# Performance work log

Measured on AMD Instinct MI355X. Metric: run time of the kernel, lower is better.

## Reference

```python
import jax, jax.numpy as jnp
import numpy as np

N = 50000   # nodes
E = 800000  # edges
D = 256     # input feature dim
H = 128     # hidden size
OUT = 40    # output classes


def setup_inputs() -> dict:
    key = jax.random.key(0)
    ks = jax.random.split(key, 10)
    s = 0.05
    return {
        "x": jax.random.normal(ks[0], (N, D), jnp.float32),
        "edge_index": jax.random.randint(ks[1], (2, E), 0, N, dtype=jnp.int64),
        "W0": jax.random.normal(ks[2], (D, H), jnp.float32) * s,
        "b0": jnp.zeros((H,), jnp.float32),
        "W1": jax.random.normal(ks[3], (H, H), jnp.float32) * s,
        "b1": jnp.zeros((H,), jnp.float32),
        "W2": jax.random.normal(ks[4], (H, H), jnp.float32) * s,
        "b2": jnp.zeros((H,), jnp.float32),
        "Wout": jax.random.normal(ks[5], (H * 3, OUT), jnp.float32) * s,
        "bout": jnp.zeros((OUT,), jnp.float32),
    }


def _gcn_norm(edge_index, n):
    # PyG gcn_norm: add self-loops, symmetric D^-1/2 (A+I) D^-1/2 weights
    row, col = edge_index[0], edge_index[1]
    loop = jnp.arange(n, dtype=edge_index.dtype)
    row = jnp.concatenate([row, loop])
    col = jnp.concatenate([col, loop])
    deg = jax.ops.segment_sum(jnp.ones_like(col, jnp.float32), col, num_segments=n)
    dinv = jnp.where(deg > 0, jax.lax.rsqrt(jnp.maximum(deg, 1.0)), 0.0)
    norm = dinv[row] * dinv[col]  # [E+N]
    return row, col, norm


def _gcn_conv(x, W, b, row, col, norm, n):
    h = x @ W                                   # dense transform first (PyG order)
    msg = h[row] * norm[:, None]                # gather source feats, scale
    out = jax.ops.segment_sum(msg, col, num_segments=n)  # scatter-aggregate
    return out + b


def reference(x, edge_index, W0, b0, W1, b1, W2, b2, Wout, bout):
    n = x.shape[0]
    row, col, norm = _gcn_norm(edge_index, n)
    x1 = jax.nn.relu(_gcn_conv(x, W0, b0, row, col, norm, n))
    x2 = jax.nn.relu(_gcn_conv(x1, W1, b1, row, col, norm, n))
    x3 = jax.nn.relu(_gcn_conv(x2, W2, b2, row, col, norm, n))
    xs = jnp.concatenate([x1, x2, x3], axis=-1)  # JumpingKnowledge 'cat'
    return xs @ Wout + bout
```

## Files before the change

kernel.cpp:

```cpp
#include <hip/hip_runtime.h>

#define HID 128
#define NOUT 40
#define SCAN_B 256

typedef __attribute__((ext_vector_type(8))) short bf16x8;
typedef __attribute__((ext_vector_type(4))) float f32x4;

__device__ inline float bf2f(unsigned short u) {
    unsigned int t = ((unsigned int)u) << 16;
    float f;
    __builtin_memcpy(&f, &t, 4);
    return f;
}
__device__ inline unsigned short f2bf(float f) {
    unsigned int x;
    __builtin_memcpy(&x, &f, 4);
    unsigned int r = (x + 0x7fffu + ((x >> 16) & 1u)) >> 16;
    return (unsigned short)r;
}
__device__ inline bf16x8 pack_bf8(float4 u, float4 v) {
    bf16x8 r;
    r[0] = (short)f2bf(u.x); r[1] = (short)f2bf(u.y);
    r[2] = (short)f2bf(u.z); r[3] = (short)f2bf(u.w);
    r[4] = (short)f2bf(v.x); r[5] = (short)f2bf(v.y);
    r[6] = (short)f2bf(v.z); r[7] = (short)f2bf(v.w);
    return r;
}

__global__ void detect_fmt_kernel(const unsigned int* __restrict__ e, int* __restrict__ flag) {
    int t = threadIdx.x;
    unsigned int v = e[2 * t + 1];
    unsigned long long ball = __ballot(v == 0u);
    if (t == 0) *flag = (ball == ~0ull) ? 1 : 0;
}

__global__ void convert_kernel(const void* __restrict__ eix, const int* __restrict__ flag,
                               int* __restrict__ rc, int* __restrict__ deg, int n2e) {
    int i = blockIdx.x * blockDim.x + threadIdx.x;
    if (i >= n2e) return;
    int f = *flag;
    int v;
    if (f) v = (int)(((const long long*)eix)[i]);
    else   v = ((const int*)eix)[i];
    rc[i] = v;
    if (i >= (n2e >> 1)) atomicAdd(&deg[v], 1);
}

__global__ void scan1_kernel(const int* __restrict__ deg, int* __restrict__ offs,
                             int* __restrict__ bsum, float* __restrict__ dinv, int N) {
    __shared__ int s[SCAN_B];
    int i = blockIdx.x * SCAN_B + threadIdx.x;
    int v = (i < N) ? deg[i] : 0;
    if (i < N) dinv[i] = rsqrtf((float)v + 1.0f);
    s[threadIdx.x] = v;
    __syncthreads();
    for (int d = 1; d < SCAN_B; d <<= 1) {
        int t = (threadIdx.x >= d) ? s[threadIdx.x - d] : 0;
        __syncthreads();
        s[threadIdx.x] += t;
        __syncthreads();
    }
    if (i < N) offs[i] = s[threadIdx.x] - v;
    if (threadIdx.x == SCAN_B - 1) bsum[blockIdx.x] = s[SCAN_B - 1];
}

__global__ void scan2_kernel(int* __restrict__ bsum, int nb) {
    __shared__ int s[SCAN_B];
    int v = (threadIdx.x < nb) ? bsum[threadIdx.x] : 0;
    s[threadIdx.x] = v;
    __syncthreads();
    for (int d = 1; d < SCAN_B; d <<= 1) {
        int t = (threadIdx.x >= d) ? s[threadIdx.x - d] : 0;
        __syncthreads();
        s[threadIdx.x] += t;
        __syncthreads();
    }
    if (threadIdx.x < nb) bsum[threadIdx.x] = s[threadIdx.x] - v;
}

__global__ void scan3_kernel(int* __restrict__ offs, const int* __restrict__ bsum,
                             int* __restrict__ cursor, int N, int E) {
    int i = blockIdx.x * SCAN_B + threadIdx.x;
    if (i < N) {
        int v = offs[i] + bsum[blockIdx.x];
        offs[i] = v;
        cursor[i] = v;
    }
    if (blockIdx.x == 0 && threadIdx.x == 0) offs[N] = E;
}

__global__ void fill_csr_kernel(const int* __restrict__ row, const int* __restrict__ col,
                                const float* __restrict__ dinv, int* __restrict__ cursor,
                                int* __restrict__ csrc, float* __restrict__ wgt, int E) {
    int e = blockIdx.x * blockDim.x + threadIdx.x;
    if (e >= E) return;
    int r = row[e];
    int c = col[e];
    int p = atomicAdd(&cursor[c], 1);
    csrc[p] = r;
    wgt[p] = dinv[r] * dinv[c];
}

__global__ void wt_kernel(const float* __restrict__ src, unsigned short* __restrict__ dst,
                          int K, int Nc, int Nr) {
    int idx = blockIdx.x * blockDim.x + threadIdx.x;
    if (idx >= Nr * K) return;
    int n = idx / K, k = idx - n * K;
    float v = (n < Nc) ? src[(size_t)k * Nc + n] : 0.f;
    dst[idx] = f2bf(v);
}

template <bool AF32>
__global__ __launch_bounds__(256) void gemm_mfma_kernel(
    const void* __restrict__ Ap, const unsigned short* __restrict__ Wt,
    unsigned short* __restrict__ H, int M, int K) {
    const int tid = threadIdx.x;
    const int lane = tid & 63;
    const int w = tid >> 6;
    const int wr = w >> 1, wc = w & 1;
    const int lr = lane & 15;
    const int ko = lane >> 4;
    const int bm = blockIdx.x * 64;

    f32x4 acc[2][4];
#pragma unroll
    for (int i = 0; i < 2; ++i)
#pragma unroll
        for (int j = 0; j < 4; ++j) acc[i][j] = (f32x4){0.f, 0.f, 0.f, 0.f};

    size_t aoff[2];
#pragma unroll
    for (int mi = 0; mi < 2; ++mi) {
        int R = bm + wr * 32 + mi * 16 + lr;
        if (R >= M) R = M - 1;
        aoff[mi] = (size_t)R * K + ko * 8;
    }
    size_t boff[4];
#pragma unroll
    for (int ni = 0; ni < 4; ++ni) {
        int n = wc * 64 + ni * 16 + lr;
        boff[ni] = (size_t)n * K + ko * 8;
    }

#pragma unroll 4
    for (int k0 = 0; k0 < K; k0 += 32) {
        bf16x8 a[2], b[4];
#pragma unroll
        for (int mi = 0; mi < 2; ++mi) {
            if constexpr (AF32) {
                const float* p = (const float*)Ap + aoff[mi] + k0;
                float4 u = *(const float4*)p;
                float4 v = *(const float4*)(p + 4);
                a[mi] = pack_bf8(u, v);
            } else {
                a[mi] = *(const bf16x8*)((const unsigned short*)Ap + aoff[mi] + k0);
            }
        }
#pragma unroll
        for (int ni = 0; ni < 4; ++ni) b[ni] = *(const bf16x8*)(Wt + boff[ni] + k0);
#pragma unroll
        for (int mi = 0; mi < 2; ++mi)
#pragma unroll
            for (int ni = 0; ni < 4; ++ni)
                acc[mi][ni] = __builtin_amdgcn_mfma_f32_16x16x32_bf16(a[mi], b[ni], acc[mi][ni], 0, 0, 0);
    }

#pragma unroll
    for (int mi = 0; mi < 2; ++mi) {
        int Rb = bm + wr * 32 + mi * 16 + ko * 4;
#pragma unroll
        for (int r = 0; r < 4; ++r) {
            int R = Rb + r;
            if (R < M) {
#pragma unroll
                for (int ni = 0; ni < 4; ++ni) {
                    int C = wc * 64 + ni * 16 + lr;
                    H[(size_t)R * HID + C] = f2bf(acc[mi][ni][r]);
                }
            }
        }
    }
}

__global__ __launch_bounds__(256) void agg_csr_kernel(
    const unsigned int* __restrict__ h32, const int* __restrict__ offs, const int* __restrict__ csrc,
    const float* __restrict__ wgt, const float* __restrict__ dinv, const float* __restrict__ bias,
    unsigned int* __restrict__ xo, int N) {
    const int lane = threadIdx.x & 63;
    const int n = (blockIdx.x * blockDim.x + threadIdx.x) >> 6;
    if (n >= N) return;
    const float d = dinv[n];
    unsigned int sv = h32[(size_t)n * 64 + lane];
    float ax = bf2f((unsigned short)(sv & 0xffff)) * (d * d) + bias[2 * lane + 0];
    float ay = bf2f((unsigned short)(sv >> 16)) * (d * d) + bias[2 * lane + 1];
    int e = offs[n];
    const int e1 = offs[n + 1];

    for (; e + 8 <= e1; e += 8) {
        int r[8];
        float wv[8];
        unsigned int v[8];
#pragma unroll
        for (int j = 0; j < 8; ++j) r[j] = csrc[e + j];
#pragma unroll
        for (int j = 0; j < 8; ++j) wv[j] = wgt[e + j];
#pragma unroll
        for (int j = 0; j < 8; ++j) v[j] = h32[(size_t)r[j] * 64 + lane];
#pragma unroll
        for (int j = 0; j < 8; ++j) {
            ax += bf2f((unsigned short)(v[j] & 0xffff)) * wv[j];
            ay += bf2f((unsigned short)(v[j] >> 16)) * wv[j];
        }
    }
    for (; e + 4 <= e1; e += 4) {
        int r[4];
        float wv[4];
        unsigned int v[4];
#pragma unroll
        for (int j = 0; j < 4; ++j) r[j] = csrc[e + j];
#pragma unroll
        for (int j = 0; j < 4; ++j) wv[j] = wgt[e + j];
#pragma unroll
        for (int j = 0; j < 4; ++j) v[j] = h32[(size_t)r[j] * 64 + lane];
#pragma unroll
        for (int j = 0; j < 4; ++j) {
            ax += bf2f((unsigned short)(v[j] & 0xffff)) * wv[j];
            ay += bf2f((unsigned short)(v[j] >> 16)) * wv[j];
        }
    }
    for (; e < e1; ++e) {
        int r = csrc[e];
        float wv = wgt[e];
        unsigned int v = h32[(size_t)r * 64 + lane];
        ax += bf2f((unsigned short)(v & 0xffff)) * wv;
        ay += bf2f((unsigned short)(v >> 16)) * wv;
    }
    ax = fmaxf(ax, 0.f);
    ay = fmaxf(ay, 0.f);
    xo[(size_t)n * 64 + lane] = (unsigned int)f2bf(ax) | ((unsigned int)f2bf(ay) << 16);
}

__global__ __launch_bounds__(256) void head_mfma_kernel(
    const unsigned short* __restrict__ x1, const unsigned short* __restrict__ x2,
    const unsigned short* __restrict__ x3, const unsigned short* __restrict__ Wt,
    const float* __restrict__ bout, float* __restrict__ out, int M) {
    const int tid = threadIdx.x;
    const int lane = tid & 63;
    const int w = tid >> 6;
    const int lr = lane & 15;
    const int ko = lane >> 4;
    const int bm = blockIdx.x * 64;
    int R = bm + w * 16 + lr;
    if (R >= M) R = M - 1;
    const unsigned short* xs[3] = {x1, x2, x3};

    f32x4 acc[3];
#pragma unroll
    for (int i = 0; i < 3; ++i) acc[i] = (f32x4){0.f, 0.f, 0.f, 0.f};

#pragma unroll
    for (int s = 0; s < 3; ++s) {
        const unsigned short* xp = xs[s] + (size_t)R * HID + ko * 8;
#pragma unroll
        for (int c = 0; c < 4; ++c) {
            bf16x8 a = *(const bf16x8*)(xp + c * 32);
#pragma unroll
            for (int ni = 0; ni < 3; ++ni) {
                bf16x8 b = *(const bf16x8*)(Wt + (size_t)(ni * 16 + lr) * 384 + s * 128 + c * 32 + ko * 8);
                acc[ni] = __builtin_amdgcn_mfma_f32_16x16x32_bf16(a, b, acc[ni], 0, 0, 0);
            }
        }
    }

    int Rb = bm + w * 16 + ko * 4;
#pragma unroll
    for (int r = 0; r < 4; ++r) {
        int Ro = Rb + r;
        if (Ro < M) {
#pragma unroll
            for (int ni = 0; ni < 3; ++ni) {
                int C = ni * 16 + lr;
                if (C < NOUT) out[(size_t)Ro * NOUT + C] = acc[ni][r] + bout[C];
            }
        }
    }
}

static inline size_t align_up(size_t x, size_t a) { return (x + a - 1) / a * a; }

extern "C" void kernel_launch(void* const* d_in, const int* in_sizes, int n_in,
                              void* d_out, int out_size, void* d_ws, size_t ws_size,
                              hipStream_t stream) {
    const float* x    = (const float*)d_in[0];
    const void*  eix  = d_in[1];
    const float* W0   = (const float*)d_in[2];
    const float* b0   = (const float*)d_in[3];
    const float* W1   = (const float*)d_in[4];
    const float* b1   = (const float*)d_in[5];
    const float* W2   = (const float*)d_in[6];
    const float* b2   = (const float*)d_in[7];
    const float* Wout = (const float*)d_in[8];
    const float* bout = (const float*)d_in[9];
    float* out = (float*)d_out;

    const int D = 256;
    const int N = in_sizes[0] / D;
    const int E = in_sizes[1] / 2;

    char* w = (char*)d_ws;
    size_t off = 0;
    int* rc = (int*)(w + off);              off = align_up(off + (size_t)2 * E * 4, 256);
    int* deg = (int*)(w + off);             off = align_up(off + (size_t)N * 4, 256);
    float* dinv = (float*)(w + off);        off = align_up(off + (size_t)N * 4, 256);
    int* offs = (int*)(w + off);            off = align_up(off + (size_t)(N + 1) * 4, 256);
    int* cursor = (int*)(w + off);          off = align_up(off + (size_t)N * 4, 256);
    int* bsum = (int*)(w + off);            off = align_up(off + 1024 * 4, 256);
    int* flag = (int*)(w + off);            off = align_up(off + 16, 256);
    int* csrc = (int*)(w + off);            off = align_up(off + (size_t)E * 4, 256);
    float* wgt = (float*)(w + off);         off = align_up(off + (size_t)E * 4, 256);
    unsigned short* h   = (unsigned short*)(w + off); off = align_up(off + (size_t)N * HID * 2, 256);
    unsigned short* x1b = (unsigned short*)(w + off); off = align_up(off + (size_t)N * HID * 2, 256);
    unsigned short* x2b = (unsigned short*)(w + off); off = align_up(off + (size_t)N * HID * 2, 256);
    unsigned short* x3b = (unsigned short*)(w + off); off = align_up(off + (size_t)N * HID * 2, 256);
    unsigned short* W0t = (unsigned short*)(w + off); off = align_up(off + (size_t)HID * 256 * 2, 256);
    unsigned short* W1t = (unsigned short*)(w + off); off = align_up(off + (size_t)HID * HID * 2, 256);
    unsigned short* W2t = (unsigned short*)(w + off); off = align_up(off + (size_t)HID * HID * 2, 256);
    unsigned short* Wot = (unsigned short*)(w + off); off = align_up(off + (size_t)48 * 384 * 2, 256);
    (void)ws_size;

    int* row = rc;
    int* col = rc + E;

    detect_fmt_kernel<<<1, 64, 0, stream>>>((const unsigned int*)eix, flag);
    hipMemsetAsync(deg, 0, (size_t)N * 4, stream);
    convert_kernel<<<(2 * E + 255) / 256, 256, 0, stream>>>(eix, flag, rc, deg, 2 * E);

    const int nb = (N + SCAN_B - 1) / SCAN_B;
    scan1_kernel<<<nb, SCAN_B, 0, stream>>>(deg, offs, bsum, dinv, N);
    scan2_kernel<<<1, SCAN_B, 0, stream>>>(bsum, nb);
    scan3_kernel<<<nb, SCAN_B, 0, stream>>>(offs, bsum, cursor, N, E);
    fill_csr_kernel<<<(E + 255) / 256, 256, 0, stream>>>(row, col, dinv, cursor, csrc, wgt, E);

    wt_kernel<<<(HID * 256 + 255) / 256, 256, 0, stream>>>(W0, W0t, 256, HID, HID);
    wt_kernel<<<(HID * HID + 255) / 256, 256, 0, stream>>>(W1, W1t, HID, HID, HID);
    wt_kernel<<<(HID * HID + 255) / 256, 256, 0, stream>>>(W2, W2t, HID, HID, HID);
    wt_kernel<<<(48 * 384 + 255) / 256, 256, 0, stream>>>(Wout, Wot, 384, NOUT, 48);

    const int gGemm = (N + 63) / 64;
    const int gAgg = (N * 64 + 255) / 256;

    gemm_mfma_kernel<true><<<gGemm, 256, 0, stream>>>(x, W0t, h, N, 256);
    agg_csr_kernel<<<gAgg, 256, 0, stream>>>((const unsigned int*)h, offs, csrc, wgt, dinv, b0, (unsigned int*)x1b, N);
    gemm_mfma_kernel<false><<<gGemm, 256, 0, stream>>>(x1b, W1t, h, N, HID);
    agg_csr_kernel<<<gAgg, 256, 0, stream>>>((const unsigned int*)h, offs, csrc, wgt, dinv, b1, (unsigned int*)x2b, N);
    gemm_mfma_kernel<false><<<gGemm, 256, 0, stream>>>(x2b, W2t, h, N, HID);
    agg_csr_kernel<<<gAgg, 256, 0, stream>>>((const unsigned int*)h, offs, csrc, wgt, dinv, b2, (unsigned int*)x3b, N);
    head_mfma_kernel<<<gGemm, 256, 0, stream>>>(x1b, x2b, x3b, Wot, bout, out, N);
}
```

Measured before the change: 400.9 us.

## Pack CSR source and weight, drop edge copy, merge weight transposes

```diff
diff --git a/kernel.cpp b/kernel.cpp
--- a/kernel.cpp
+++ b/kernel.cpp
@@ -7,8 +7,8 @@
 typedef __attribute__((ext_vector_type(8))) short bf16x8;
 typedef __attribute__((ext_vector_type(4))) float f32x4;
 
-__device__ inline float bf2f(unsigned short u) {
-    unsigned int t = ((unsigned int)u) << 16;
+__device__ inline float bf2f(unsigned int u) {
+    unsigned int t = u << 16;
     float f;
     __builtin_memcpy(&f, &t, 4);
     return f;
@@ -35,16 +35,13 @@
     if (t == 0) *flag = (ball == ~0ull) ? 1 : 0;
 }
 
-__global__ void convert_kernel(const void* __restrict__ eix, const int* __restrict__ flag,
-                               int* __restrict__ rc, int* __restrict__ deg, int n2e) {
+__global__ void degree_kernel(const void* __restrict__ eix, const int* __restrict__ flag,
+                              int* __restrict__ deg, int E) {
     int i = blockIdx.x * blockDim.x + threadIdx.x;
-    if (i >= n2e) return;
+    if (i >= E) return;
     int f = *flag;
-    int v;
-    if (f) v = (int)(((const long long*)eix)[i]);
-    else   v = ((const int*)eix)[i];
-    rc[i] = v;
-    if (i >= (n2e >> 1)) atomicAdd(&deg[v], 1);
+    int c = f ? (int)(((const long long*)eix)[(size_t)E + i]) : ((const int*)eix)[(size_t)E + i];
+    atomicAdd(&deg[c], 1);
 }
 
 __global__ void scan1_kernel(const int* __restrict__ deg, int* __restrict__ offs,
@@ -90,25 +87,47 @@
     if (blockIdx.x == 0 && threadIdx.x == 0) offs[N] = E;
 }
 
-__global__ void fill_csr_kernel(const int* __restrict__ row, const int* __restrict__ col,
+__global__ void fill_csr_kernel(const void* __restrict__ eix, const int* __restrict__ flag,
                                 const float* __restrict__ dinv, int* __restrict__ cursor,
-                                int* __restrict__ csrc, float* __restrict__ wgt, int E) {
+                                int2* __restrict__ pkd, int E) {
     int e = blockIdx.x * blockDim.x + threadIdx.x;
     if (e >= E) return;
-    int r = row[e];
-    int c = col[e];
+    int f = *flag;
+    int r, c;
+    if (f) {
+        r = (int)(((const long long*)eix)[e]);
+        c = (int)(((const long long*)eix)[(size_t)E + e]);
+    } else {
+        r = ((const int*)eix)[e];
+        c = ((const int*)eix)[(size_t)E + e];
+    }
     int p = atomicAdd(&cursor[c], 1);
-    csrc[p] = r;
-    wgt[p] = dinv[r] * dinv[c];
-}
-
-__global__ void wt_kernel(const float* __restrict__ src, unsigned short* __restrict__ dst,
-                          int K, int Nc, int Nr) {
+    float wv = dinv[r] * dinv[c];
+    int2 rec;
+    rec.x = r;
+    rec.y = __float_as_int(wv);
+    pkd[p] = rec;
+}
+
+__global__ void wt_all_kernel(const float* __restrict__ W0, const float* __restrict__ W1,
+                              const float* __restrict__ W2, const float* __restrict__ Wo,
+                              unsigned short* __restrict__ W0t, unsigned short* __restrict__ W1t,
+                              unsigned short* __restrict__ W2t, unsigned short* __restrict__ Wot) {
     int idx = blockIdx.x * blockDim.x + threadIdx.x;
-    if (idx >= Nr * K) return;
-    int n = idx / K, k = idx - n * K;
-    float v = (n < Nc) ? src[(size_t)k * Nc + n] : 0.f;
-    dst[idx] = f2bf(v);
+    const int s0 = 128 * 256, s1 = 128 * 128, s2 = 128 * 128, s3 = 48 * 384;
+    if (idx < s0) {
+        int n = idx >> 8, k = idx & 255;
+        W0t[idx] = f2bf(W0[(size_t)k * 128 + n]);
+    } else if ((idx -= s0) < s1) {
+        int n = idx >> 7, k = idx & 127;
+        W1t[idx] = f2bf(W1[(size_t)k * 128 + n]);
+    } else if ((idx -= s1) < s2) {
+        int n = idx >> 7, k = idx & 127;
+        W2t[idx] = f2bf(W2[(size_t)k * 128 + n]);
+    } else if ((idx -= s2) < s3) {
+        int n = idx / 384, k = idx - n * 384;
+        Wot[idx] = (n < NOUT) ? f2bf(Wo[(size_t)k * NOUT + n]) : (unsigned short)0;
+    }
 }
 
 template <bool AF32>
@@ -184,57 +203,53 @@
 }
 
 __global__ __launch_bounds__(256) void agg_csr_kernel(
-    const unsigned int* __restrict__ h32, const int* __restrict__ offs, const int* __restrict__ csrc,
-    const float* __restrict__ wgt, const float* __restrict__ dinv, const float* __restrict__ bias,
-    unsigned int* __restrict__ xo, int N) {
+    const unsigned int* __restrict__ h32, const int* __restrict__ offs,
+    const int2* __restrict__ pkd, const float* __restrict__ dinv,
+    const float* __restrict__ bias, unsigned int* __restrict__ xo, int N) {
     const int lane = threadIdx.x & 63;
     const int n = (blockIdx.x * blockDim.x + threadIdx.x) >> 6;
     if (n >= N) return;
     const float d = dinv[n];
     unsigned int sv = h32[(size_t)n * 64 + lane];
-    float ax = bf2f((unsigned short)(sv & 0xffff)) * (d * d) + bias[2 * lane + 0];
-    float ay = bf2f((unsigned short)(sv >> 16)) * (d * d) + bias[2 * lane + 1];
+    float ax = bf2f(sv & 0xffff) * (d * d) + bias[2 * lane + 0];
+    float ay = bf2f(sv >> 16) * (d * d) + bias[2 * lane + 1];
     int e = offs[n];
     const int e1 = offs[n + 1];
 
-    for (; e + 8 <= e1; e += 8) {
-        int r[8];
-        float wv[8];
-        unsigned int v[8];
-#pragma unroll
-        for (int j = 0; j < 8; ++j) r[j] = csrc[e + j];
-#pragma unroll
-        for (int j = 0; j < 8; ++j) wv[j] = wgt[e + j];
-#pragma unroll
-        for (int j = 0; j < 8; ++j) v[j] = h32[(size_t)r[j] * 64 + lane];
-#pragma unroll
-        for (int j = 0; j < 8; ++j) {
-            ax += bf2f((unsigned short)(v[j] & 0xffff)) * wv[j];
-            ay += bf2f((unsigned short)(v[j] >> 16)) * wv[j];
+    for (; e + 16 <= e1; e += 16) {
+        int2 pk[16];
+        unsigned int v[16];
+#pragma unroll
+        for (int j = 0; j < 16; ++j) pk[j] = pkd[e + j];
+#pragma unroll
+        for (int j = 0; j < 16; ++j) v[j] = h32[(size_t)pk[j].x * 64 + lane];
+#pragma unroll
+        for (int j = 0; j < 16; ++j) {
+            float wv = __int_as_float(pk[j].y);
+            ax += bf2f(v[j] & 0xffff) * wv;
+            ay += bf2f(v[j] >> 16) * wv;
         }
     }
     for (; e + 4 <= e1; e += 4) {
-        int r[4];
-        float wv[4];
+        int2 pk[4];
         unsigned int v[4];
 #pragma unroll
-        for (int j = 0; j < 4; ++j) r[j] = csrc[e + j];
-#pragma unroll
-        for (int j = 0; j < 4; ++j) wv[j] = wgt[e + j];
-#pragma unroll
-        for (int j = 0; j < 4; ++j) v[j] = h32[(size_t)r[j] * 64 + lane];
+        for (int j = 0; j < 4; ++j) pk[j] = pkd[e + j];
+#pragma unroll
+        for (int j = 0; j < 4; ++j) v[j] = h32[(size_t)pk[j].x * 64 + lane];
 #pragma unroll
         for (int j = 0; j < 4; ++j) {
-            ax += bf2f((unsigned short)(v[j] & 0xffff)) * wv[j];
-            ay += bf2f((unsigned short)(v[j] >> 16)) * wv[j];
+            float wv = __int_as_float(pk[j].y);
+            ax += bf2f(v[j] & 0xffff) * wv;
+            ay += bf2f(v[j] >> 16) * wv;
         }
     }
     for (; e < e1; ++e) {
-        int r = csrc[e];
-        float wv = wgt[e];
-        unsigned int v = h32[(size_t)r * 64 + lane];
-        ax += bf2f((unsigned short)(v & 0xffff)) * wv;
-        ay += bf2f((unsigned short)(v >> 16)) * wv;
+        int2 pk = pkd[e];
+        unsigned int v = h32[(size_t)pk.x * 64 + lane];
+        float wv = __int_as_float(pk.y);
+        ax += bf2f(v & 0xffff) * wv;
+        ay += bf2f(v >> 16) * wv;
     }
     ax = fmaxf(ax, 0.f);
     ay = fmaxf(ay, 0.f);
@@ -310,15 +325,13 @@
 
     char* w = (char*)d_ws;
     size_t off = 0;
-    int* rc = (int*)(w + off);              off = align_up(off + (size_t)2 * E * 4, 256);
     int* deg = (int*)(w + off);             off = align_up(off + (size_t)N * 4, 256);
     float* dinv = (float*)(w + off);        off = align_up(off + (size_t)N * 4, 256);
     int* offs = (int*)(w + off);            off = align_up(off + (size_t)(N + 1) * 4, 256);
     int* cursor = (int*)(w + off);          off = align_up(off + (size_t)N * 4, 256);
     int* bsum = (int*)(w + off);            off = align_up(off + 1024 * 4, 256);
     int* flag = (int*)(w + off);            off = align_up(off + 16, 256);
-    int* csrc = (int*)(w + off);            off = align_up(off + (size_t)E * 4, 256);
-    float* wgt = (float*)(w + off);         off = align_up(off + (size_t)E * 4, 256);
+    int2* pkd = (int2*)(w + off);           off = align_up(off + (size_t)E * 8, 256);
     unsigned short* h   = (unsigned short*)(w + off); off = align_up(off + (size_t)N * HID * 2, 256);
     unsigned short* x1b = (unsigned short*)(w + off); off = align_up(off + (size_t)N * HID * 2, 256);
     unsigned short* x2b = (unsigned short*)(w + off); off = align_up(off + (size_t)N * HID * 2, 256);
@@ -329,32 +342,27 @@
     unsigned short* Wot = (unsigned short*)(w + off); off = align_up(off + (size_t)48 * 384 * 2, 256);
     (void)ws_size;
 
-    int* row = rc;
-    int* col = rc + E;
-
     detect_fmt_kernel<<<1, 64, 0, stream>>>((const unsigned int*)eix, flag);
     hipMemsetAsync(deg, 0, (size_t)N * 4, stream);
-    convert_kernel<<<(2 * E + 255) / 256, 256, 0, stream>>>(eix, flag, rc, deg, 2 * E);
+    degree_kernel<<<(E + 255) / 256, 256, 0, stream>>>(eix, flag, deg, E);
 
     const int nb = (N + SCAN_B - 1) / SCAN_B;
     scan1_kernel<<<nb, SCAN_B, 0, stream>>>(deg, offs, bsum, dinv, N);
     scan2_kernel<<<1, SCAN_B, 0, stream>>>(bsum, nb);
     scan3_kernel<<<nb, SCAN_B, 0, stream>>>(offs, bsum, cursor, N, E);
-    fill_csr_kernel<<<(E + 255) / 256, 256, 0, stream>>>(row, col, dinv, cursor, csrc, wgt, E);
-
-    wt_kernel<<<(HID * 256 + 255) / 256, 256, 0, stream>>>(W0, W0t, 256, HID, HID);
-    wt_kernel<<<(HID * HID + 255) / 256, 256, 0, stream>>>(W1, W1t, HID, HID, HID);
-    wt_kernel<<<(HID * HID + 255) / 256, 256, 0, stream>>>(W2, W2t, HID, HID, HID);
-    wt_kernel<<<(48 * 384 + 255) / 256, 256, 0, stream>>>(Wout, Wot, 384, NOUT, 48);
+    fill_csr_kernel<<<(E + 255) / 256, 256, 0, stream>>>(eix, flag, dinv, cursor, pkd, E);
+
+    const int wtTot = 128 * 256 + 128 * 128 + 128 * 128 + 48 * 384;
+    wt_all_kernel<<<(wtTot + 255) / 256, 256, 0, stream>>>(W0, W1, W2, Wout, W0t, W1t, W2t, Wot);
 
     const int gGemm = (N + 63) / 64;
     const int gAgg = (N * 64 + 255) / 256;
 
     gemm_mfma_kernel<true><<<gGemm, 256, 0, stream>>>(x, W0t, h, N, 256);
-    agg_csr_kernel<<<gAgg, 256, 0, stream>>>((const unsigned int*)h, offs, csrc, wgt, dinv, b0, (unsigned int*)x1b, N);
+    agg_csr_kernel<<<gAgg, 256, 0, stream>>>((const unsigned int*)h, offs, pkd, dinv, b0, (unsigned int*)x1b, N);
     gemm_mfma_kernel<false><<<gGemm, 256, 0, stream>>>(x1b, W1t, h, N, HID);
-    agg_csr_kernel<<<gAgg, 256, 0, stream>>>((const unsigned int*)h, offs, csrc, wgt, dinv, b1, (unsigned int*)x2b, N);
+    agg_csr_kernel<<<gAgg, 256, 0, stream>>>((const unsigned int*)h, offs, pkd, dinv, b1, (unsigned int*)x2b, N);
     gemm_mfma_kernel<false><<<gGemm, 256, 0, stream>>>(x2b, W2t, h, N, HID);
-    agg_csr_kernel<<<gAgg, 256, 0, stream>>>((const unsigned int*)h, offs, csrc, wgt, dinv, b2, (unsigned int*)x3b, N);
+    agg_csr_kernel<<<gAgg, 256, 0, stream>>>((const unsigned int*)h, offs, pkd, dinv, b2, (unsigned int*)x3b, N);
     head_mfma_kernel<<<gGemm, 256, 0, stream>>>(x1b, x2b, x3b, Wot, bout, out, N);
 }
```

After: 390.4 us. 2.6% less time.
